# Kernel tuning notes

Measured on AMD Instinct MI355X. Metric: run time of the kernel, lower is better.

The kernel has to match this reference:

```python
import jax, jax.numpy as jnp
import numpy as np
from jax import lax

WINDOW_SIZE = 11
CHANNEL = 3
SIGMA = 1.5
C1 = 0.01 ** 2
C2 = 0.03 ** 2


def _create_window(window_size: int, channel: int) -> jnp.ndarray:
    g = jnp.arange(window_size, dtype=jnp.float32)
    g = jnp.exp(-(g - window_size // 2) ** 2 / (2.0 * SIGMA ** 2))
    g = g / g.sum()
    w2d = g[:, None] * g[None, :]                      # (K, K)
    # HWIO layout for grouped (depthwise) conv: (K, K, 1, channel)
    return jnp.tile(w2d[:, :, None, None], (1, 1, 1, channel))


def _dwconv(x: jnp.ndarray, window: jnp.ndarray) -> jnp.ndarray:
    pad = WINDOW_SIZE // 2
    return lax.conv_general_dilated(
        x, window,
        window_strides=(1, 1),
        padding=((pad, pad), (pad, pad)),
        dimension_numbers=("NCHW", "HWIO", "NCHW"),
        feature_group_count=CHANNEL,
    )


def setup_inputs() -> dict:
    key = jax.random.key(0)
    k1, k2 = jax.random.split(key)
    shape = (16, 3, 512, 512)
    img1 = jax.random.uniform(k1, shape, dtype=jnp.float32)
    img2 = jax.random.uniform(k2, shape, dtype=jnp.float32)
    window = _create_window(WINDOW_SIZE, CHANNEL)
    return {"img1": img1, "img2": img2, "window": window}


def reference(img1, img2, window):
    mu1 = _dwconv(img1, window)
    mu2 = _dwconv(img2, window)
    mu1_sq = mu1 * mu1
    mu2_sq = mu2 * mu2
    mu1_mu2 = mu1 * mu2
    sigma1_sq = _dwconv(img1 * img1, window) - mu1_sq
    sigma2_sq = _dwconv(img2 * img2, window) - mu2_sq
    sigma12 = _dwconv(img1 * img2, window) - mu1_mu2
    ssim_map = ((2.0 * mu1_mu2 + C1) * (2.0 * sigma12 + C2)) / (
        (mu1_sq + mu2_sq + C1) * (sigma1_sq + sigma2_sq + C2)
    )
    return ssim_map.mean()  # size_average=True
```

## Files before the change

kernel.cpp:

```cpp
#include <hip/hip_runtime.h>

#define KW 11
#define PAD 5
#define TW 64
#define TH 32
#define HROWS 16
#define ICOLS 74
#define S4 77
#define SX 77
#define IMH 512
#define IMW 512
#define NBLK 6144

typedef float f2 __attribute__((ext_vector_type(2)));
typedef float f4 __attribute__((ext_vector_type(4)));


#define A_LOAD(EDGE_, H_)                                                     \
    if (aon) {                                                                \
        const int gr0 = iy0 + (H_) * HROWS + ar0;                             \
        if (EDGE_) {                                                          \
            const bool cok = (agc >= 0) && (agc < IMW);                       \
            _Pragma("unroll")                                                 \
            for (int i = 0; i < 14; ++i) {                                    \
                const int gr = gr0 + i;                                       \
                const bool ok = cok && (gr >= 0) && (gr < IMH);               \
                const size_t o = base + (size_t)(ok ? gr : 0) * IMW           \
                               + (ok ? agc : 0);                              \
                p1[i] = ok ? img1[o] : 0.f;                                   \
                p2[i] = ok ? img2[o] : 0.f;                                   \
            }                                                                 \
        } else {                                                              \
                   \
            _Pragma("unroll")                                                 \
            for (int i = 0; i < 14; ++i) {                                    \
                const size_t o = base + (size_t)(gr0 + i) * IMW + agc;        \
                p1[i] = img1[o];                                              \
                p2[i] = img2[o];                                              \
            }                                                                 \
        }                                                                     \
    }

#define A_CONV(H_)                                                            \
    if (aon) {                                                                \
        f2 m12[4]  = {{0,0},{0,0},{0,0},{0,0}};                               \
        f2 qq[4]   = {{0,0},{0,0},{0,0},{0,0}};                               \
        f2 sx01 = {0, 0}, sx23 = {0, 0};                                      \
        _Pragma("unroll")                                                     \
        for (int i = 0; i < 14; ++i) {                                        \
            f2 x12; x12.x = p1[i]; x12.y = p2[i];                             \
            const f2 sq = x12 * x12;                                          \
            const float sxy = p1[i] * p2[i];                                  \
            f2 sxy2; sxy2.x = sxy; sxy2.y = sxy;                              \
            _Pragma("unroll")                                                 \
            for (int k = 0; k < 4; ++k) {                                     \
                const int j = i - k;                                          \
                if (j >= 0 && j < KW) {                                       \
                    const float w = wg[j];                  \
                    const f2 w2 = {w, w};                                     \
                    m12[k] += w2 * x12;                     \
                    qq[k]  += w2 * sq;                      \
                }                                                             \
            }                                                                 \
            if (i >= 1 && i <= 10)       sx01 += wp[i] * sxy2;                \
            else if (i == 0)             sx01.x += wg[0]  * sxy;              \
            else if (i == 11)            sx01.y += wg[10] * sxy;              \
            if (i >= 3 && i <= 12)       sx23 += wp[i - 2] * sxy2;            \
            else if (i == 2)             sx23.x += wg[0]  * sxy;              \
            else if (i == 13)            sx23.y += wg[10] * sxy;              \
        }                                                                     \
        const float sxs[4] = {sx01.x, sx01.y, sx23.x, sx23.y};                \
        _Pragma("unroll")                                                     \
        for (int k = 0; k < 4; ++k) {                                         \
            f4 v;                                                             \
            v.x = m12[k].x; v.y = m12[k].y;                                   \
            v.z = qq[k].x;  v.w = qq[k].y;                                    \
            vv4[(ar0 + k) * S4 + ac] = v;                  \
            vsx[(ar0 + k) * SX + ac] = sxs[k];             \
        }                                                                     \
    }

#define PHASE_B(H_)                                                           \
    {                                                                         \
        const int row = t & 15;                                               \
        const int cp  = t >> 4;                                    \
        const f4* __restrict__ p4 = &vv4[row * S4 + cp * 2];                  \
        const float* __restrict__ px = &vsx[row * SX + cp * 2];               \
        f2 am12[2] = {{0,0},{0,0}};                                           \
        f2 aqq[2]  = {{0,0},{0,0}};                                           \
        f2 asxp = {0, 0};                                                     \
        _Pragma("unroll")                                                     \
        for (int b = 0; b < 3; ++b) {                                         \
            f4 v[4]; float vx[4];                                             \
            _Pragma("unroll")                                                 \
            for (int cc = 0; cc < 4; ++cc) {                                  \
                v[cc]  = p4[b * 4 + cc];                                      \
                vx[cc] = px[b * 4 + cc];                                      \
            }                                                                 \
            _Pragma("unroll")                                                 \
            for (int cc = 0; cc < 4; ++cc) {                                  \
                const int cg = b * 4 + cc;                                    \
                f2 v12; v12.x = v[cc].x; v12.y = v[cc].y;                     \
                f2 vqq; vqq.x = v[cc].z; vqq.y = v[cc].w;                     \
                _Pragma("unroll")                                             \
                for (int k = 0; k < 2; ++k) {                                 \
                    const int j = cg - k;                                     \
                    if (j >= 0 && j < KW) {                                   \
                        const float w = wg[j];                                \
                        const f2 w2 = {w, w};                                 \
                        am12[k] += w2 * v12;                                  \
                        aqq[k]  += w2 * vqq;                                  \
                    }                                                         \
                }                                                             \
                f2 vx2; vx2.x = vx[cc]; vx2.y = vx[cc];                       \
                if (cg >= 1 && cg <= 10)  asxp += wp[cg] * vx2;               \
                else if (cg == 0)         asxp.x += wg[0]  * vx[cc];          \
                else if (cg == 11)        asxp.y += wg[10] * vx[cc];          \
            }                                                                 \
        }                                                                     \
        const float asx[2] = {asxp.x, asxp.y};                                \
        _Pragma("unroll")                                                     \
        for (int k = 0; k < 2; ++k) {                                         \
            const float mu1 = am12[k].x, mu2 = am12[k].y;                     \
            const float mu1sq = mu1 * mu1, mu2sq = mu2 * mu2;                 \
            const float mu12 = mu1 * mu2;                                     \
            const float sig1 = aqq[k].x - mu1sq;                              \
            const float sig2 = aqq[k].y - mu2sq;                              \
            const float sig12 = asx[k] - mu12;                                \
            const float num = (2.f * mu12 + C1v) * (2.f * sig12 + C2v);       \
            const float den = (mu1sq + mu2sq + C1v) * (sig1 + sig2 + C2v);    \
            float r = __builtin_amdgcn_rcpf(den);                             \
            r = r * (2.f - den * r);               \
            lsum += num * r;                                                  \
        }                                                                     \
    }

__global__ __launch_bounds__(512, 4) void ssim_main(
    const float* __restrict__ img1, const float* __restrict__ img2,
    const float* __restrict__ window, float* __restrict__ partial)
{
    __shared__ f4 vv4[HROWS * S4];
    __shared__ float vsx[HROWS * SX];
    __shared__ float g[KW];
    __shared__ float wsum[8];

    const int t = threadIdx.x;

    const int plane = blockIdx.z;
    const size_t base = (size_t)plane * IMH * IMW;
    const int ix0 = blockIdx.x * TW - PAD;
    const int iy0 = blockIdx.y * TH - PAD;

    const bool aon = t < ICOLS * 4;
    const int ac  = t % ICOLS;
    const int ar0 = (t / ICOLS) * 4;
    const int agc = ix0 + ac;

    const bool interior = (ix0 >= 0) && (ix0 + ICOLS <= IMW) &&
                          (iy0 >= 0) && (iy0 + TH + KW - 1 <= IMH);

    float p1[14], p2[14];

    if (interior) { A_LOAD(false, 0) } else { A_LOAD(true, 0) }

    if (t < KW) {
        float s = 0.f;
        for (int j = 0; j < KW; ++j) s += window[(t * KW + j) * 3];
        g[t] = s;
    }
    __syncthreads();

    float wg[KW];
#pragma unroll
    for (int j = 0; j < KW; ++j) {
        const int bi = __builtin_amdgcn_readfirstlane(__float_as_int(g[j]));
        wg[j] = __int_as_float(bi);
    }
    f2 wp[KW];
#pragma unroll
    for (int j = 1; j < KW; ++j) { wp[j].x = wg[j]; wp[j].y = wg[j - 1]; }

    const float C1v = 0.0001f;
    const float C2v = 0.0009f;
    float lsum = 0.f;

    A_CONV(0)
    __syncthreads();

    if (interior) { A_LOAD(false, 1) } else { A_LOAD(true, 1) }
    PHASE_B(0)
    __syncthreads();

    A_CONV(1)
    __syncthreads();
    PHASE_B(1)

#pragma unroll
    for (int off = 32; off > 0; off >>= 1) lsum += __shfl_down(lsum, off, 64);
    if ((t & 63) == 0) wsum[t >> 6] = lsum;
    __syncthreads();
    if (t == 0) {
        float bs = 0.f;
#pragma unroll
        for (int w = 0; w < 8; ++w) bs += wsum[w];
        unsigned bid = (blockIdx.z * gridDim.y + blockIdx.y) * gridDim.x
                     + blockIdx.x;
        partial[bid] = bs;
    }
}

__global__ __launch_bounds__(1024) void ssim_reduce(
    const float* __restrict__ partial, float* __restrict__ out, double inv_n)
{
    __shared__ double dsum[16];
    const int t = threadIdx.x;
    double s = 0.0;
    for (int i = t; i < NBLK; i += 1024) s += (double)partial[i];
#pragma unroll
    for (int off = 32; off > 0; off >>= 1) s += __shfl_down(s, off, 64);
    if ((t & 63) == 0) dsum[t >> 6] = s;
    __syncthreads();
    if (t == 0) {
        double tot = 0.0;
#pragma unroll
        for (int w = 0; w < 16; ++w) tot += dsum[w];
        out[0] = (float)(tot * inv_n);
    }
}

extern "C" void kernel_launch(void* const* d_in, const int* in_sizes, int n_in,
                              void* d_out, int out_size, void* d_ws, size_t ws_size,
                              hipStream_t stream) {
    const float* img1   = (const float*)d_in[0];
    const float* img2   = (const float*)d_in[1];
    const float* window = (const float*)d_in[2];
    float* out = (float*)d_out;
    float* partial = (float*)d_ws;

    const int nplanes = in_sizes[0] / (IMH * IMW);
    const long long total = (long long)in_sizes[0];

    dim3 grid(IMW / TW, IMH / TH, nplanes);
    ssim_main<<<grid, 512, 0, stream>>>(img1, img2, window, partial);
    ssim_reduce<<<1, 1024, 0, stream>>>(partial, out, 1.0 / (double)total);
}
```

Measured before the change: 161.3 us.

## Stage second-half input rows into LDS via otherwise idle threads

Threads beyond the convolution workers (t>=320) now prefetch the second half-tile's raw input rows for both images into a new interleaved shared buffer at kernel start. This happens while the first half is loaded and convolved, so the global load of half 1 no longer sits between the two phases. The second vertical pass then reads pairs from LDS instead of registers loaded from global. The cost is extra shared memory (about 15 KB), which may reduce occupancy, plus per-element index division in the staging loop.

After: 159.0 us. Within noise of the previous version (-1.4%).

```diff
diff --git a/kernel.cpp b/kernel.cpp
--- a/kernel.cpp
+++ b/kernel.cpp
@@ -11,14 +11,20 @@
 #define IMH 512
 #define IMW 512
 #define NBLK 6144
+#define NCONV 296
+#define LBASE 320
+#define NLOAD 192
+#define RAWROWS 26
+#define RAWV (2*RAWROWS*74)
+#define LTASK 21
 
 typedef float f2 __attribute__((ext_vector_type(2)));
 typedef float f4 __attribute__((ext_vector_type(4)));
 
 
-#define A_LOAD(EDGE_, H_)                                                     \
-    if (aon) {                                                                \
-        const int gr0 = iy0 + (H_) * HROWS + ar0;                             \
+#define A_LOAD(EDGE_)                                                         \
+    if (t < NCONV) {                                                          \
+        const int gr0 = iy0 + ar0;                                            \
         if (EDGE_) {                                                          \
             const bool cok = (agc >= 0) && (agc < IMW);                       \
             _Pragma("unroll")                                                 \
@@ -31,7 +37,6 @@
                 p2[i] = ok ? img2[o] : 0.f;                                   \
             }                                                                 \
         } else {                                                              \
-                   \
             _Pragma("unroll")                                                 \
             for (int i = 0; i < 14; ++i) {                                    \
                 const size_t o = base + (size_t)(gr0 + i) * IMW + agc;        \
@@ -41,16 +46,40 @@
         }                                                                     \
     }
 
-#define A_CONV(H_)                                                            \
-    if (aon) {                                                                \
+#define RAW_STAGE(EDGE_)                                                      \
+    {                                                                         \
+        float rv[LTASK];                                                      \
+        _Pragma("unroll")                                                     \
+        for (int s = 0; s < LTASK; ++s) {                                     \
+            const int o = lidx + NLOAD * s;                                   \
+            const int row = o / 148;                                          \
+            const int col = (o % 148) >> 1;                                   \
+            const int gr = iy1 + row;            \
+            const int gc = ix0 + col;                                         \
+            const float* sp = (o & 1) ? img2 : img1;                          \
+            bool ok = (s != LTASK - 1) || (o < RAWV);                         \
+            if (EDGE_) ok = ok && (gr < IMH) && (gc >= 0) && (gc < IMW);      \
+            const size_t go = base + (size_t)(ok ? gr : 0) * IMW              \
+                            + (ok ? gc : 0);                                  \
+            rv[s] = ok ? sp[go] : 0.f;                                        \
+        }                                                                     \
+        _Pragma("unroll")                                                     \
+        for (int s = 0; s < LTASK; ++s) {                                     \
+            const int o = lidx + NLOAD * s;                                   \
+            if (s != LTASK - 1 || o < RAWV) raw[o] = rv[s];                   \
+        }                                                                     \
+    }
+
+#define A_CONV_BODY(GETX_)                                                    \
+    {                                                                         \
         f2 m12[4]  = {{0,0},{0,0},{0,0},{0,0}};                               \
         f2 qq[4]   = {{0,0},{0,0},{0,0},{0,0}};                               \
         f2 sx01 = {0, 0}, sx23 = {0, 0};                                      \
         _Pragma("unroll")                                                     \
         for (int i = 0; i < 14; ++i) {                                        \
-            f2 x12; x12.x = p1[i]; x12.y = p2[i];                             \
+            f2 x12; GETX_;                                                    \
             const f2 sq = x12 * x12;                                          \
-            const float sxy = p1[i] * p2[i];                                  \
+            const float sxy = x12.x * x12.y;                                  \
             f2 sxy2; sxy2.x = sxy; sxy2.y = sxy;                              \
             _Pragma("unroll")                                                 \
             for (int k = 0; k < 4; ++k) {                                     \
@@ -141,6 +170,7 @@
 {
     __shared__ f4 vv4[HROWS * S4];
     __shared__ float vsx[HROWS * SX];
+    __shared__ __align__(16) float raw[RAWV];
     __shared__ float g[KW];
     __shared__ float wsum[8];
 
@@ -150,18 +180,23 @@
     const size_t base = (size_t)plane * IMH * IMW;
     const int ix0 = blockIdx.x * TW - PAD;
     const int iy0 = blockIdx.y * TH - PAD;
-
-    const bool aon = t < ICOLS * 4;
+    const int iy1 = iy0 + HROWS;
+
     const int ac  = t % ICOLS;
     const int ar0 = (t / ICOLS) * 4;
     const int agc = ix0 + ac;
+    const int lidx = t - LBASE;
 
     const bool interior = (ix0 >= 0) && (ix0 + ICOLS <= IMW) &&
                           (iy0 >= 0) && (iy0 + TH + KW - 1 <= IMH);
 
     float p1[14], p2[14];
 
-    if (interior) { A_LOAD(false, 0) } else { A_LOAD(true, 0) }
+    if (t < LBASE) {
+        if (interior) { A_LOAD(false) } else { A_LOAD(true) }
+    } else {
+        if (interior) { RAW_STAGE(false) } else { RAW_STAGE(true) }
+    }
 
     if (t < KW) {
         float s = 0.f;
@@ -184,15 +219,17 @@
     const float C2v = 0.0009f;
     float lsum = 0.f;
 
-    A_CONV(0)
-    __syncthreads();
-
-    if (interior) { A_LOAD(false, 1) } else { A_LOAD(true, 1) }
+    if (t < NCONV) A_CONV_BODY(x12.x = p1[i]; x12.y = p2[i];)
+    __syncthreads();
+
     PHASE_B(0)
     __syncthreads();
 
-    A_CONV(1)
-    __syncthreads();
+    if (t < NCONV)
+        A_CONV_BODY(x12 = *reinterpret_cast<const f2*>(
+                        &raw[((ar0 + i) * 74 + ac) * 2]);)
+    __syncthreads();
+
     PHASE_B(1)
 
 #pragma unroll
```
